# Performance work log

Hardware: AMD Instinct MI355X
Metric: run time of the kernel (lower is better)

## Reference

```python
import jax, jax.numpy as jnp
import numpy as np


def _box_filter(x, k):
    """Mean filter with border-count normalization (count_include_pad=False).
    x: [B, C, H, W] float. Returns same shape.
    """
    B, C, H, W = x.shape
    pad = (k - 1) // 2
    ones_k = jnp.ones((1, 1, k, k), dtype=x.dtype)
    # Sum over kxk window with zero padding: treat channels as batch.
    xs = x.reshape(B * C, 1, H, W)
    win_sum = jax.lax.conv_general_dilated(
        xs, ones_k, window_strides=(1, 1), padding=[(pad, pad), (pad, pad)],
        dimension_numbers=("NCHW", "OIHW", "NCHW"))
    win_sum = win_sum.reshape(B, C, H, W)
    # Count of valid (in-bounds) taps per output pixel; independent of B, C.
    ones_img = jnp.ones((1, 1, H, W), dtype=x.dtype)
    counts = jax.lax.conv_general_dilated(
        ones_img, ones_k, window_strides=(1, 1), padding=[(pad, pad), (pad, pad)],
        dimension_numbers=("NCHW", "OIHW", "NCHW"))  # [1,1,H,W]
    return win_sum / counts


def setup_inputs() -> dict:
    key = jax.random.key(0)
    x = jax.random.normal(key, (32, 3, 512, 512), dtype=jnp.float32)
    return {"x": x, "k_size": 5}


def reference(x, k_size):
    return _box_filter(x, k_size)
```

## Files before the change

kernel.cpp:

```cpp
#include <hip/hip_runtime.h>


#define HH 512
#define WW 512
#define NPLANES 96
#define SROWS 8
#define STRIPS (HH / SROWS)
#define NROWS (SROWS + 4)

__global__ __launch_bounds__(64, 2) void box5_kernel(const float* __restrict__ x,
                                                     float* __restrict__ out) {
    const int lane = threadIdx.x;
    const int gid = blockIdx.x;
    const int plane = gid / STRIPS;
    const int strip = gid % STRIPS;
    const int y0 = strip * SROWS;

    const float* px = x + (size_t)plane * (HH * WW);
    float* pout = out + (size_t)plane * (HH * WW);
    const int w0 = lane * 8;

    float4 ra[NROWS], rb[NROWS];
#pragma unroll
    for (int r = 0; r < NROWS; ++r) {
        int y = y0 - 2 + r;
        int yc = min(max(y, 0), HH - 1);
        const float* p = px + (size_t)yc * WW + w0;
        ra[r] = *(const float4*)(p);
        rb[r] = *(const float4*)(p + 4);
    }

    float hs[NROWS][8];
#pragma unroll
    for (int r = 0; r < NROWS; ++r) {
        const int y = y0 - 2 + r;
        const float mask = (y >= 0 && y < HH) ? 1.0f : 0.0f;

        const float xv0 = ra[r].x, xv1 = ra[r].y, xv2 = ra[r].z, xv3 = ra[r].w;
        const float xv4 = rb[r].x, xv5 = rb[r].y, xv6 = rb[r].z, xv7 = rb[r].w;

        float xm2 = __shfl_up(xv6, 1);
        float xm1 = __shfl_up(xv7, 1);
        float xp1 = __shfl_down(xv0, 1);
        float xp2 = __shfl_down(xv1, 1);
        if (lane == 0)  { xm2 = 0.0f; xm1 = 0.0f; }
        if (lane == 63) { xp1 = 0.0f; xp2 = 0.0f; }

        float t = xm2 + xm1 + xv0 + xv1 + xv2;
        hs[r][0] = t;
        t += xv3 - xm2; hs[r][1] = t;
        t += xv4 - xm1; hs[r][2] = t;
        t += xv5 - xv0; hs[r][3] = t;
        t += xv6 - xv1; hs[r][4] = t;
        t += xv7 - xv2; hs[r][5] = t;
        t += xp1 - xv3; hs[r][6] = t;
        t += xp2 - xv4; hs[r][7] = t;
#pragma unroll
        for (int j = 0; j < 8; ++j) hs[r][j] *= mask;
    }

    float inv_cw[8];
#pragma unroll
    for (int j = 0; j < 8; ++j) {
        int w = w0 + j;
        int cw = min(w + 2, WW - 1) - max(w - 2, 0) + 1;
        inv_cw[j] = 1.0f / (float)cw;
    }

#pragma unroll
    for (int o = 0; o < SROWS; ++o) {
        const int y_out = y0 + o;
        const int ch = min(y_out + 2, HH - 1) - max(y_out - 2, 0) + 1;
        const float inv_ch = 1.0f / (float)ch;

        float ov[8];
#pragma unroll
        for (int j = 0; j < 8; ++j) {
            float vs = hs[o][j] + hs[o + 1][j] + hs[o + 2][j] + hs[o + 3][j] + hs[o + 4][j];
            ov[j] = vs * (inv_cw[j] * inv_ch);
        }
        float* po = pout + (size_t)y_out * WW + w0;
        *(float4*)(po)     = make_float4(ov[0], ov[1], ov[2], ov[3]);
        *(float4*)(po + 4) = make_float4(ov[4], ov[5], ov[6], ov[7]);
    }
}

extern "C" void kernel_launch(void* const* d_in, const int* in_sizes, int n_in,
                              void* d_out, int out_size, void* d_ws, size_t ws_size,
                              hipStream_t stream) {
    const float* x = (const float*)d_in[0];
    float* out = (float*)d_out;
    dim3 grid(NPLANES * STRIPS);
    box5_kernel<<<grid, 64, 0, stream>>>(x, out);
}
```

Baseline: 187.1 us.

## Stage row tile in LDS via direct global-to-LDS loads with 256-thread blocks

Each block now covers a 16-row strip with four waves and 256 threads. The 20 input rows are staged into shared memory with asynchronous global_load_lds transfers, then each wave reads 8 rows from LDS to produce 4 output rows. This is meant to raise occupancy and the number of bytes in flight, and to cut halo re-reads compared with 64-thread, 8-row strips. In exchange it uses 40KB of LDS per block, which caps how many blocks fit per CU, and adds a block-wide barrier.

```diff
diff --git a/kernel.cpp b/kernel.cpp
--- a/kernel.cpp
+++ b/kernel.cpp
@@ -4,40 +4,63 @@
 #define HH 512
 #define WW 512
 #define NPLANES 96
-#define SROWS 8
+#define SROWS 16
 #define STRIPS (HH / SROWS)
-#define NROWS (SROWS + 4)
+#define TROWS (SROWS + 4)
+#define NCHUNK (TROWS * 2)
 
-__global__ __launch_bounds__(64, 2) void box5_kernel(const float* __restrict__ x,
-                                                     float* __restrict__ out) {
-    const int lane = threadIdx.x;
-    const int gid = blockIdx.x;
+typedef const __attribute__((address_space(1))) void* gas_ptr;
+typedef __attribute__((address_space(3))) void* las_ptr;
+
+__global__ __launch_bounds__(256, 4) void box5_kernel(const float* __restrict__ x,
+                                                      float* __restrict__ out) {
+    __shared__ float smem[TROWS * WW];
+
+    const int tid  = threadIdx.x;
+    const int lane = tid & 63;
+    const int wv   = tid >> 6;
+    const int gid  = blockIdx.x;
     const int plane = gid / STRIPS;
     const int strip = gid % STRIPS;
     const int y0 = strip * SROWS;
 
     const float* px = x + (size_t)plane * (HH * WW);
     float* pout = out + (size_t)plane * (HH * WW);
+
+#pragma unroll
+    for (int i = 0; i < NCHUNK / 4; ++i) {
+        const int idx  = wv * (NCHUNK / 4) + i;
+        const int r    = idx >> 1;
+        const int half = idx & 1;
+        const int yc = min(max(y0 - 2 + r, 0), HH - 1);
+        const float* gsrc = px + (size_t)yc * WW + half * (WW / 2) + lane * 4;
+        __builtin_amdgcn_global_load_lds((gas_ptr)gsrc,
+                                         (las_ptr)&smem[r * WW + half * (WW / 2)],
+                                         16, 0, 0);
+    }
+    __syncthreads();
+
     const int w0 = lane * 8;
 
-    float4 ra[NROWS], rb[NROWS];
+    float inv_cw[8];
 #pragma unroll
-    for (int r = 0; r < NROWS; ++r) {
-        int y = y0 - 2 + r;
-        int yc = min(max(y, 0), HH - 1);
-        const float* p = px + (size_t)yc * WW + w0;
-        ra[r] = *(const float4*)(p);
-        rb[r] = *(const float4*)(p + 4);
+    for (int j = 0; j < 8; ++j) {
+        int w = w0 + j;
+        int cw = min(w + 2, WW - 1) - max(w - 2, 0) + 1;
+        inv_cw[j] = 1.0f / (float)cw;
     }
 
-    float hs[NROWS][8];
+    float hs[8][8];
 #pragma unroll
-    for (int r = 0; r < NROWS; ++r) {
-        const int y = y0 - 2 + r;
+    for (int q = 0; q < 8; ++q) {
+        const int lr = wv * 4 + q;
+        const int y  = y0 - 2 + lr;
         const float mask = (y >= 0 && y < HH) ? 1.0f : 0.0f;
 
-        const float xv0 = ra[r].x, xv1 = ra[r].y, xv2 = ra[r].z, xv3 = ra[r].w;
-        const float xv4 = rb[r].x, xv5 = rb[r].y, xv6 = rb[r].z, xv7 = rb[r].w;
+        const float4 a = *(const float4*)&smem[lr * WW + w0];
+        const float4 b = *(const float4*)&smem[lr * WW + w0 + 4];
+        const float xv0 = a.x, xv1 = a.y, xv2 = a.z, xv3 = a.w;
+        const float xv4 = b.x, xv5 = b.y, xv6 = b.z, xv7 = b.w;
 
         float xm2 = __shfl_up(xv6, 1);
         float xm1 = __shfl_up(xv7, 1);
@@ -47,29 +70,21 @@
         if (lane == 63) { xp1 = 0.0f; xp2 = 0.0f; }
 
         float t = xm2 + xm1 + xv0 + xv1 + xv2;
-        hs[r][0] = t;
-        t += xv3 - xm2; hs[r][1] = t;
-        t += xv4 - xm1; hs[r][2] = t;
-        t += xv5 - xv0; hs[r][3] = t;
-        t += xv6 - xv1; hs[r][4] = t;
-        t += xv7 - xv2; hs[r][5] = t;
-        t += xp1 - xv3; hs[r][6] = t;
-        t += xp2 - xv4; hs[r][7] = t;
+        hs[q][0] = t;
+        t += xv3 - xm2; hs[q][1] = t;
+        t += xv4 - xm1; hs[q][2] = t;
+        t += xv5 - xv0; hs[q][3] = t;
+        t += xv6 - xv1; hs[q][4] = t;
+        t += xv7 - xv2; hs[q][5] = t;
+        t += xp1 - xv3; hs[q][6] = t;
+        t += xp2 - xv4; hs[q][7] = t;
 #pragma unroll
-        for (int j = 0; j < 8; ++j) hs[r][j] *= mask;
-    }
-
-    float inv_cw[8];
-#pragma unroll
-    for (int j = 0; j < 8; ++j) {
-        int w = w0 + j;
-        int cw = min(w + 2, WW - 1) - max(w - 2, 0) + 1;
-        inv_cw[j] = 1.0f / (float)cw;
+        for (int j = 0; j < 8; ++j) hs[q][j] *= mask;
     }
 
 #pragma unroll
-    for (int o = 0; o < SROWS; ++o) {
-        const int y_out = y0 + o;
+    for (int o = 0; o < 4; ++o) {
+        const int y_out = y0 + wv * 4 + o;
         const int ch = min(y_out + 2, HH - 1) - max(y_out - 2, 0) + 1;
         const float inv_ch = 1.0f / (float)ch;
 
@@ -91,5 +106,5 @@
     const float* x = (const float*)d_in[0];
     float* out = (float*)d_out;
     dim3 grid(NPLANES * STRIPS);
-    box5_kernel<<<grid, 64, 0, stream>>>(x, out);
+    box5_kernel<<<grid, 256, 0, stream>>>(x, out);
 }
```

Measured after the change: 178.0 us. 4.9% less time.
